# Kernel optimization log

Hardware: AMD Instinct MI355X
Metric: run time of the kernel (lower is better)

The kernel has to match this reference:

```python
import jax, jax.numpy as jnp
import numpy as np

DIST_THRESHOLD = 3.33  # threshold on SQUARED distances (pytorch3d knn_points.dists are squared)


def setup_inputs() -> dict:
    key = jax.random.key(0)
    k1, k2, k3, k4, k5, k6 = jax.random.split(key, 6)
    B, N, D = 4, 8192, 3
    points_src = jax.random.normal(k1, (B, N, D), dtype=jnp.float32)
    points_dst = jax.random.normal(k2, (B, N, D), dtype=jnp.float32)
    flows_pred = jax.random.normal(k3, (B, N, D), dtype=jnp.float32)
    flows_gt = jax.random.normal(k4, (B, N, D), dtype=jnp.float32)
    masks_src = jax.random.randint(k5, (B, N), 0, 2, dtype=jnp.int32)
    masks_dst = jax.random.randint(k6, (B, N), 0, 2, dtype=jnp.int32)
    return {"points_src": points_src, "points_dst": points_dst,
            "flows_pred": flows_pred, "flows_gt": flows_gt,
            "masks_src": masks_src, "masks_dst": masks_dst}


def _pairwise_sq_dists(a, b):
    # a: [N,3], b: [M,3] -> [N,M] squared euclidean distances via gram trick
    a2 = jnp.sum(a * a, axis=-1)  # [N]
    b2 = jnp.sum(b * b, axis=-1)  # [M]
    d2 = a2[:, None] + b2[None, :] - 2.0 * (a @ b.T)
    return jnp.maximum(d2, 0.0)


def _chamfer_thresholded(pw, pd, ms, md):
    # pw: warped src points [N,3]; pd: dst points [M,3]; ms/md: validity masks (>0)
    valid_s = ms > 0  # [N]
    valid_d = md > 0  # [M]
    d2 = _pairwise_sq_dists(pw, pd)  # [N,M]
    # K=1 NN in each direction; invalid points in the *search* set get +inf
    d_wt = jnp.min(jnp.where(valid_d[None, :], d2, jnp.inf), axis=1)  # [N]
    d_tw = jnp.min(jnp.where(valid_s[:, None], d2, jnp.inf), axis=0)  # [M]
    # thresholded mean over valid query points (mirrors boolean-index + .mean())
    sel_wt = valid_s & (d_wt < DIST_THRESHOLD)
    sel_tw = valid_d & (d_tw < DIST_THRESHOLD)
    mean_wt = jnp.sum(jnp.where(sel_wt, d_wt, 0.0)) / jnp.sum(sel_wt)
    mean_tw = jnp.sum(jnp.where(sel_tw, d_tw, 0.0)) / jnp.sum(sel_tw)
    return mean_wt + mean_tw


def reference(points_src, points_dst, flows_pred, flows_gt, masks_src, masks_dst):
    points_src_warped = points_src + flows_pred  # [B,N,3]
    per_sample = jax.vmap(_chamfer_thresholded)(points_src_warped, points_dst,
                                                masks_src, masks_dst)  # [B]
    return jnp.sum(per_sample)
```

## Files before the change

### kernel.cpp

```cpp
#include <hip/hip_runtime.h>
#include <hip/hip_bf16.h>

#define NPTS 8192
#define NB   4
#define BLK  256
#define NREG 32
#define QPT  4
#define QPB  (QPT * BLK)
#define NQC_MAX (NPTS / QPB)
#define NSL  32
#define SMAX ((NPTS + NSL - 1) / NSL)
#define CAP  NPTS
#define THR  3.33f

#define OFF_PSUM 4096
#define OFF_PCNT 8192
#define OFF_BEST 16384
#define OFF_PTS  (16384 + 8 * CAP * 4)

__device__ __forceinline__ unsigned enc_f(float f) {
    unsigned u = __float_as_uint(f);
    return (u & 0x80000000u) ? ~u : (u | 0x80000000u);
}
__device__ __forceinline__ float dec_f(unsigned u) {
    return (u & 0x80000000u) ? __uint_as_float(u & 0x7FFFFFFFu)
                             : __uint_as_float(~u);
}

__device__ __forceinline__ void build_prefix(const unsigned* __restrict__ bcnt,
                                             int qi, int* P, int tid) {
    if (tid < 64) {
        const int lane = tid & 63;
        int v = (lane < NREG) ? (int)bcnt[qi * NREG + lane] : 0;
#pragma unroll
        for (int o = 1; o < NREG; o <<= 1) {
            int t = __shfl_up(v, o);
            if (lane >= o) v += t;
        }
        if (lane < NREG) P[lane + 1] = v;
        if (lane == 0) P[0] = 0;
    }
}

__device__ __forceinline__ int map_region(const int* P, int id) {
    int r = 0;
#pragma unroll
    for (int s = 16; s; s >>= 1)
        if (P[r + s] <= id) r += s;
    return r;
}

__global__ __launch_bounds__(BLK) void compact_kernel(
    const float* __restrict__ Ps, const float* __restrict__ Pd,
    const float* __restrict__ F,  const int* __restrict__ Ms,
    const int* __restrict__ Md,   unsigned* __restrict__ bcnt,
    float4* __restrict__ pts,     unsigned* __restrict__ best)
{
    const int b = blockIdx.z, side = blockIdx.y, r = blockIdx.x;
    const int qi = b * 2 + side;
    const int tid = threadIdx.x;
    const int g = b * NPTS + r * BLK + tid;

    best[(size_t)qi * CAP + r * BLK + tid] = 0u;

    float x, y, z; int v;
    if (side == 0) {
        x = Ps[3 * g + 0] + F[3 * g + 0];
        y = Ps[3 * g + 1] + F[3 * g + 1];
        z = Ps[3 * g + 2] + F[3 * g + 2];
        v = Ms[g];
    } else {
        x = Pd[3 * g + 0]; y = Pd[3 * g + 1]; z = Pd[3 * g + 2];
        v = Md[g];
    }
    const bool valid = v > 0;

    const int lane = tid & 63, w = tid >> 6;
    unsigned long long m = __ballot(valid);
    const int my = __popcll(m & ((1ull << lane) - 1ull));
    __shared__ int wc[4];
    if (lane == 0) wc[w] = __popcll(m);
    __syncthreads();
    int off = 0;
#pragma unroll
    for (int i = 0; i < 4; ++i) if (i < w) off += wc[i];
    if (valid)
        pts[(size_t)qi * CAP + r * BLK + off + my] =
            make_float4(2.f * x, 2.f * y, 2.f * z, -(x * x + y * y + z * z));
    if (tid == 0)
        bcnt[qi * NREG + r] = (unsigned)(wc[0] + wc[1] + wc[2] + wc[3]);
}

__global__ __launch_bounds__(BLK) void knn_kernel(
    const unsigned* __restrict__ bcnt, const float4* __restrict__ pts,
    unsigned* __restrict__ best)
{
    const int b = blockIdx.z, d = blockIdx.y;
    const int qc = blockIdx.x / NSL, sl = blockIdx.x % NSL;
    const int qi = b * 2 + d;
    const int si = b * 2 + (1 - d);
    const int tid = threadIdx.x;

    __shared__ int Pq[NREG + 1], Psx[NREG + 1];
    __shared__ float4 sp[SMAX];

    if (tid < 64) {
        const int lane = tid & 63;
        int vq = (lane < NREG) ? (int)bcnt[qi * NREG + lane] : 0;
        int vs = (lane < NREG) ? (int)bcnt[si * NREG + lane] : 0;
#pragma unroll
        for (int o = 1; o < NREG; o <<= 1) {
            int tq = __shfl_up(vq, o);
            int ts = __shfl_up(vs, o);
            if (lane >= o) { vq += tq; vs += ts; }
        }
        if (lane < NREG) { Pq[lane + 1] = vq; Psx[lane + 1] = vs; }
        if (lane == 0) { Pq[0] = 0; Psx[0] = 0; }
    }
    __syncthreads();

    const int nq = Pq[NREG], ns = Psx[NREG];
    if (qc * QPB >= nq) return;
    const int L = (ns + NSL - 1) / NSL;
    const int start = sl * L;
    int len = ns - start; if (len > L) len = L;
    if (len <= 0) return;

    if (tid < len) {
        const int id = start + tid;
        const int r = map_region(Psx, id);
        sp[tid] = pts[(size_t)si * CAP + r * BLK + (id - Psx[r])];
    }
    __syncthreads();

    float qx[QPT], qy[QPT], qz[QPT], bt[QPT];
    bool qv[QPT]; int qn[QPT];
#pragma unroll
    for (int k = 0; k < QPT; ++k) {
        const int q = qc * QPB + k * BLK + tid;
        qn[k] = q; qv[k] = q < nq;
        const int qq = qv[k] ? q : 0;
        const int r = map_region(Pq, qq);
        const float4 p = pts[(size_t)qi * CAP + r * BLK + (qq - Pq[r])];
        qx[k] = 0.5f * p.x; qy[k] = 0.5f * p.y; qz[k] = 0.5f * p.z;
        bt[k] = -1e30f;
    }

#pragma unroll 4
    for (int j = 0; j < len; ++j) {
        const float4 s = sp[j];
#pragma unroll
        for (int k = 0; k < QPT; ++k) {
            float t = fmaf(qx[k], s.x, s.w);
            t = fmaf(qy[k], s.y, t);
            t = fmaf(qz[k], s.z, t);
            bt[k] = fmaxf(bt[k], t);
        }
    }

#pragma unroll
    for (int k = 0; k < QPT; ++k)
        if (qv[k])
            atomicMax(&best[(size_t)qi * CAP + qn[k]], enc_f(bt[k]));
}

__global__ __launch_bounds__(BLK) void finalize_kernel(
    const unsigned* __restrict__ bcnt, const float4* __restrict__ pts,
    const unsigned* __restrict__ best, float* __restrict__ psum,
    float* __restrict__ pcnt)
{
    const int b = blockIdx.z, side = blockIdx.y, bx = blockIdx.x;
    const int qi = b * 2 + side;
    const int tid = threadIdx.x;

    __shared__ int Pq[NREG + 1];
    build_prefix(bcnt, qi, Pq, tid);
    __syncthreads();

    const int nq = Pq[NREG];
    const int q = bx * BLK + tid;
    float s = 0.f, c = 0.f;
    if (q < nq) {
        const int r = map_region(Pq, q);
        const float4 p = pts[(size_t)qi * CAP + r * BLK + (q - Pq[r])];
        const float t = dec_f(best[(size_t)qi * CAP + q]);
        float dd = fmaxf((-p.w) - t, 0.f);
        if (dd < THR) { s = dd; c = 1.f; }
    }
#pragma unroll
    for (int off = 32; off; off >>= 1) {
        s += __shfl_down(s, off);
        c += __shfl_down(c, off);
    }
    __shared__ float red[8];
    const int w = tid >> 6;
    if ((tid & 63) == 0) { red[w] = s; red[4 + w] = c; }
    __syncthreads();
    if (tid == 0) {
        psum[qi * NREG + bx] = red[0] + red[1] + red[2] + red[3];
        pcnt[qi * NREG + bx] = red[4] + red[5] + red[6] + red[7];
    }
}

__global__ void reduce_out_kernel(const float* __restrict__ psum,
                                  const float* __restrict__ pcnt,
                                  float* __restrict__ out)
{
    const int tid = threadIdx.x;
    float a = 0.f;
    if (tid < 8) {
        float s = 0.f, c = 0.f;
        for (int r = 0; r < NREG; ++r) {
            s += psum[tid * NREG + r];
            c += pcnt[tid * NREG + r];
        }
        a = s / c;
    }
#pragma unroll
    for (int off = 4; off; off >>= 1) a += __shfl_down(a, off);
    if (tid == 0) out[0] = a;
}

extern "C" void kernel_launch(void* const* d_in, const int* in_sizes, int n_in,
                              void* d_out, int out_size, void* d_ws, size_t ws_size,
                              hipStream_t stream)
{
    const float* Ps = (const float*)d_in[0];
    const float* Pd = (const float*)d_in[1];
    const float* F  = (const float*)d_in[2];
    const int* Ms = (const int*)d_in[4];
    const int* Md = (const int*)d_in[5];
    float* out = (float*)d_out;

    unsigned* bcnt = (unsigned*)d_ws;
    float* psum = (float*)((char*)d_ws + OFF_PSUM);
    float* pcnt = (float*)((char*)d_ws + OFF_PCNT);
    unsigned* best = (unsigned*)((char*)d_ws + OFF_BEST);
    float4* pts = (float4*)((char*)d_ws + OFF_PTS);

    compact_kernel<<<dim3(NREG, 2, NB), BLK, 0, stream>>>(
        Ps, Pd, F, Ms, Md, bcnt, pts, best);

    knn_kernel<<<dim3(NQC_MAX * NSL, 2, NB), BLK, 0, stream>>>(bcnt, pts, best);

    finalize_kernel<<<dim3(NREG, 2, NB), BLK, 0, stream>>>(
        bcnt, pts, best, psum, pcnt);

    reduce_out_kernel<<<1, 64, 0, stream>>>(psum, pcnt, out);
}
```

Measured before the change: 33.97 us.

## Replace atomicMax with per-slice partial maxima and fuse final reduction

The KNN kernel no longer does atomicMax into an encoded best array. Each source slice now writes its per-query maxima into a dedicated partial buffer, and the final kernel takes the max over the 32 slices while computing the thresholded sums. The separate reduce kernel is folded into the final kernel using last-block-done atomic counters. The inner loop also prefetches the next shared-memory point behind a sentinel entry. This removes about two million global atomics and one kernel launch, at the cost of writing and re-reading a roughly 8 MB partial buffer.

```diff
diff --git a/kernel.cpp b/kernel.cpp
--- a/kernel.cpp
+++ b/kernel.cpp
@@ -5,27 +5,19 @@
 #define NB   4
 #define BLK  256
 #define NREG 32
-#define QPT  4
-#define QPB  (QPT * BLK)
-#define NQC_MAX (NPTS / QPB)
+#define CAP  NPTS
+#define QPB  1024
+#define NQC  (NPTS / QPB)
 #define NSL  32
-#define SMAX ((NPTS + NSL - 1) / NSL)
-#define CAP  NPTS
+#define SMAX 257
 #define THR  3.33f
 
-#define OFF_PSUM 4096
-#define OFF_PCNT 8192
-#define OFF_BEST 16384
-#define OFF_PTS  (16384 + 8 * CAP * 4)
-
-__device__ __forceinline__ unsigned enc_f(float f) {
-    unsigned u = __float_as_uint(f);
-    return (u & 0x80000000u) ? ~u : (u | 0x80000000u);
-}
-__device__ __forceinline__ float dec_f(unsigned u) {
-    return (u & 0x80000000u) ? __uint_as_float(u & 0x7FFFFFFFu)
-                             : __uint_as_float(~u);
-}
+#define OFF_BCNT 4096
+#define OFF_PSUM 8192
+#define OFF_PCNT 12288
+#define OFF_PART 16384
+#define OFF_PTS  (16384 + 8 * NSL * NPTS * 4)
+
 
 __device__ __forceinline__ void build_prefix(const unsigned* __restrict__ bcnt,
                                              int qi, int* P, int tid) {
@@ -54,14 +46,15 @@
     const float* __restrict__ Ps, const float* __restrict__ Pd,
     const float* __restrict__ F,  const int* __restrict__ Ms,
     const int* __restrict__ Md,   unsigned* __restrict__ bcnt,
-    float4* __restrict__ pts,     unsigned* __restrict__ best)
+    float4* __restrict__ pts,     unsigned* __restrict__ ctl)
 {
     const int b = blockIdx.z, side = blockIdx.y, r = blockIdx.x;
     const int qi = b * 2 + side;
     const int tid = threadIdx.x;
     const int g = b * NPTS + r * BLK + tid;
 
-    best[(size_t)qi * CAP + r * BLK + tid] = 0u;
+    if (r == 0 && side == 0 && b == 0)
+        for (int i = tid; i < 512; i += BLK) ctl[i] = 0;
 
     float x, y, z; int v;
     if (side == 0) {
@@ -93,7 +86,7 @@
 
 __global__ __launch_bounds__(BLK) void knn_kernel(
     const unsigned* __restrict__ bcnt, const float4* __restrict__ pts,
-    unsigned* __restrict__ best)
+    float* __restrict__ part)
 {
     const int b = blockIdx.z, d = blockIdx.y;
     const int qc = blockIdx.x / NSL, sl = blockIdx.x % NSL;
@@ -131,14 +124,15 @@
         const int r = map_region(Psx, id);
         sp[tid] = pts[(size_t)si * CAP + r * BLK + (id - Psx[r])];
     }
-    __syncthreads();
-
-    float qx[QPT], qy[QPT], qz[QPT], bt[QPT];
-    bool qv[QPT]; int qn[QPT];
-#pragma unroll
-    for (int k = 0; k < QPT; ++k) {
+    if (tid == 0) sp[len] = make_float4(0.f, 0.f, 0.f, -1e30f);
+    __syncthreads();
+
+    float qx[4], qy[4], qz[4], bt[4];
+    bool qv[4];
+#pragma unroll
+    for (int k = 0; k < 4; ++k) {
         const int q = qc * QPB + k * BLK + tid;
-        qn[k] = q; qv[k] = q < nq;
+        qv[k] = q < nq;
         const int qq = qv[k] ? q : 0;
         const int r = map_region(Pq, qq);
         const float4 p = pts[(size_t)qi * CAP + r * BLK + (qq - Pq[r])];
@@ -146,46 +140,55 @@
         bt[k] = -1e30f;
     }
 
-#pragma unroll 4
+    float4 cur = sp[0];
+#pragma unroll 2
     for (int j = 0; j < len; ++j) {
-        const float4 s = sp[j];
-#pragma unroll
-        for (int k = 0; k < QPT; ++k) {
-            float t = fmaf(qx[k], s.x, s.w);
-            t = fmaf(qy[k], s.y, t);
-            t = fmaf(qz[k], s.z, t);
+        const float4 nxt = sp[j + 1];
+#pragma unroll
+        for (int k = 0; k < 4; ++k) {
+            float t = fmaf(qx[k], cur.x, cur.w);
+            t = fmaf(qy[k], cur.y, t);
+            t = fmaf(qz[k], cur.z, t);
             bt[k] = fmaxf(bt[k], t);
         }
-    }
-
-#pragma unroll
-    for (int k = 0; k < QPT; ++k)
-        if (qv[k])
-            atomicMax(&best[(size_t)qi * CAP + qn[k]], enc_f(bt[k]));
-}
-
-__global__ __launch_bounds__(BLK) void finalize_kernel(
+        cur = nxt;
+    }
+
+    float* pb = part + ((size_t)qi * NSL + sl) * NPTS + qc * QPB;
+#pragma unroll
+    for (int k = 0; k < 4; ++k)
+        if (qv[k]) pb[k * BLK + tid] = bt[k];
+}
+
+__global__ __launch_bounds__(BLK) void final_kernel(
     const unsigned* __restrict__ bcnt, const float4* __restrict__ pts,
-    const unsigned* __restrict__ best, float* __restrict__ psum,
-    float* __restrict__ pcnt)
-{
-    const int b = blockIdx.z, side = blockIdx.y, bx = blockIdx.x;
-    const int qi = b * 2 + side;
-    const int tid = threadIdx.x;
+    const float* __restrict__ part, unsigned* __restrict__ ctl,
+    float* __restrict__ out)
+{
+    const int b = blockIdx.z, dir = blockIdx.y, qc = blockIdx.x;
+    const int qi = b * 2 + dir;
+    const int tid = threadIdx.x, lane = tid & 63, w = tid >> 6;
 
     __shared__ int Pq[NREG + 1];
     build_prefix(bcnt, qi, Pq, tid);
     __syncthreads();
-
     const int nq = Pq[NREG];
-    const int q = bx * BLK + tid;
+
+    const float* pp = part + (size_t)qi * NSL * NPTS + qc * QPB;
     float s = 0.f, c = 0.f;
-    if (q < nq) {
-        const int r = map_region(Pq, q);
-        const float4 p = pts[(size_t)qi * CAP + r * BLK + (q - Pq[r])];
-        const float t = dec_f(best[(size_t)qi * CAP + q]);
-        float dd = fmaxf((-p.w) - t, 0.f);
-        if (dd < THR) { s = dd; c = 1.f; }
+#pragma unroll
+    for (int k = 0; k < 4; ++k) {
+        const int q = qc * QPB + k * BLK + tid;
+        if (q < nq) {
+            const int r = map_region(Pq, q);
+            const float4 p = pts[(size_t)qi * CAP + r * BLK + (q - Pq[r])];
+            float m = -1e30f;
+#pragma unroll
+            for (int sl = 0; sl < NSL; ++sl)
+                m = fmaxf(m, pp[(size_t)sl * NPTS + k * BLK + tid]);
+            const float dd = fmaxf((-p.w) - m, 0.f);
+            if (dd < THR) { s += dd; c += 1.f; }
+        }
     }
 #pragma unroll
     for (int off = 32; off; off >>= 1) {
@@ -193,32 +196,35 @@
         c += __shfl_down(c, off);
     }
     __shared__ float red[8];
-    const int w = tid >> 6;
-    if ((tid & 63) == 0) { red[w] = s; red[4 + w] = c; }
+    if (lane == 0) { red[w] = s; red[4 + w] = c; }
     __syncthreads();
     if (tid == 0) {
-        psum[qi * NREG + bx] = red[0] + red[1] + red[2] + red[3];
-        pcnt[qi * NREG + bx] = red[4] + red[5] + red[6] + red[7];
-    }
-}
-
-__global__ void reduce_out_kernel(const float* __restrict__ psum,
-                                  const float* __restrict__ pcnt,
-                                  float* __restrict__ out)
-{
-    const int tid = threadIdx.x;
-    float a = 0.f;
-    if (tid < 8) {
-        float s = 0.f, c = 0.f;
-        for (int r = 0; r < NREG; ++r) {
-            s += psum[tid * NREG + r];
-            c += pcnt[tid * NREG + r];
-        }
-        a = s / c;
-    }
-#pragma unroll
-    for (int off = 4; off; off >>= 1) a += __shfl_down(a, off);
-    if (tid == 0) out[0] = a;
+        float* psum  = (float*)((char*)ctl + OFF_PSUM  - 0) + 0;
+        float* pcnt_ = (float*)((char*)ctl + OFF_PCNT);
+        float* psum_ = (float*)((char*)ctl + OFF_PSUM);
+        float* meanv = (float*)(ctl + 288);
+        (void)psum;
+        psum_[qi * NQC + qc] = red[0] + red[1] + red[2] + red[3];
+        pcnt_[qi * NQC + qc] = red[4] + red[5] + red[6] + red[7];
+        const unsigned r = __hip_atomic_fetch_add(&ctl[qi * 32], 1u,
+                              __ATOMIC_ACQ_REL, __HIP_MEMORY_SCOPE_AGENT);
+        if (r == NQC - 1) {
+            float S = 0.f, C = 0.f;
+            for (int g = 0; g < NQC; ++g) {
+                S += psum_[qi * NQC + g];
+                C += pcnt_[qi * NQC + g];
+            }
+            meanv[qi] = S / C;
+            const unsigned r2 = __hip_atomic_fetch_add(&ctl[256], 1u,
+                                   __ATOMIC_ACQ_REL, __HIP_MEMORY_SCOPE_AGENT);
+            if (r2 == 2 * NB - 1) {
+                float a = 0.f;
+#pragma unroll
+                for (int i = 0; i < 2 * NB; ++i) a += meanv[i];
+                out[0] = a;
+            }
+        }
+    }
 }
 
 extern "C" void kernel_launch(void* const* d_in, const int* in_sizes, int n_in,
@@ -232,19 +238,16 @@
     const int* Md = (const int*)d_in[5];
     float* out = (float*)d_out;
 
-    unsigned* bcnt = (unsigned*)d_ws;
-    float* psum = (float*)((char*)d_ws + OFF_PSUM);
-    float* pcnt = (float*)((char*)d_ws + OFF_PCNT);
-    unsigned* best = (unsigned*)((char*)d_ws + OFF_BEST);
+    unsigned* ctl = (unsigned*)d_ws;
+    unsigned* bcnt = (unsigned*)((char*)d_ws + OFF_BCNT);
+    float* part = (float*)((char*)d_ws + OFF_PART);
     float4* pts = (float4*)((char*)d_ws + OFF_PTS);
 
     compact_kernel<<<dim3(NREG, 2, NB), BLK, 0, stream>>>(
-        Ps, Pd, F, Ms, Md, bcnt, pts, best);
-
-    knn_kernel<<<dim3(NQC_MAX * NSL, 2, NB), BLK, 0, stream>>>(bcnt, pts, best);
-
-    finalize_kernel<<<dim3(NREG, 2, NB), BLK, 0, stream>>>(
-        bcnt, pts, best, psum, pcnt);
-
-    reduce_out_kernel<<<1, 64, 0, stream>>>(psum, pcnt, out);
-}
+        Ps, Pd, F, Ms, Md, bcnt, pts, ctl);
+
+    knn_kernel<<<dim3(NQC * NSL, 2, NB), BLK, 0, stream>>>(bcnt, pts, part);
+
+    final_kernel<<<dim3(NQC, 2, NB), BLK, 0, stream>>>(
+        bcnt, pts, part, ctl, out);
+}
```

Result: slower. 41.54 us (+22.3%).
